# Kernel optimization log

Measured on AMD Instinct MI355X. Metric: run time of the kernel, lower is better.

## Reference

```python
import jax, jax.numpy as jnp
import numpy as np

B, L, D_IN = 8, 512, 1024
HEAD_SIZE = 64
NUM_LABELS = 16
INF = 1e12


def _rotary_sin_cos(seq_len, dim):
    # HF RoFormerSinusoidalPositionalEmbedding: inv_freq = 10000^(-2i/dim)
    pos = np.arange(seq_len, dtype=np.float64)[:, None]
    inv_freq = 1.0 / np.power(10000.0, 2.0 * np.arange(dim // 2) / dim)
    ang = pos * inv_freq  # [L, dim//2]
    # interleave: [s0, s0, s1, s1, ...] (matches stack([sin,sin],-1).reshape)
    sin = jnp.asarray(np.repeat(np.sin(ang), 2, axis=-1), dtype=jnp.float32)
    cos = jnp.asarray(np.repeat(np.cos(ang), 2, axis=-1), dtype=jnp.float32)
    return sin[None], cos[None]  # [1, L, dim]


def _rotate_half(x):
    # [-x1, x0, -x3, x2, ...]
    return jnp.stack([-x[..., 1::2], x[..., ::2]], axis=-1).reshape(x.shape)


def setup_inputs() -> dict:
    key = jax.random.key(0)
    k1, k2, k3, k4, k5 = jax.random.split(key, 5)
    s1 = 1.0 / np.sqrt(D_IN)
    s2 = 1.0 / np.sqrt(2 * HEAD_SIZE)
    return {
        "inputs": jax.random.normal(k1, (B, L, D_IN), dtype=jnp.float32),
        "attention_mask": jnp.ones((B, L), dtype=jnp.int32),
        "W1": jax.random.uniform(k2, (D_IN, 2 * HEAD_SIZE), jnp.float32, -s1, s1),
        "b1": jax.random.uniform(k3, (2 * HEAD_SIZE,), jnp.float32, -s1, s1),
        "W2": jax.random.uniform(k4, (2 * HEAD_SIZE, 2 * NUM_LABELS), jnp.float32, -s2, s2),
        "b2": jax.random.uniform(k5, (2 * NUM_LABELS,), jnp.float32, -s2, s2),
    }


def reference(inputs, attention_mask, W1, b1, W2, b2):
    h = inputs @ W1 + b1                      # [B, L, 2*head_size]
    qw, kw = h[..., ::2], h[..., 1::2]        # [B, L, head_size]

    sin, cos = _rotary_sin_cos(h.shape[1], HEAD_SIZE)
    qw = qw * cos + _rotate_half(qw) * sin
    kw = kw * cos + _rotate_half(kw) * sin

    logits = jnp.einsum("bmd,bnd->bmn", qw, kw) / (HEAD_SIZE ** 0.5)  # [B, L, L]

    bias = (h @ W2 + b2).transpose(0, 2, 1) / 2.0        # [B, 2*heads, L]
    logits = logits[:, None] + bias[:, ::2, None, :] + bias[:, 1::2, :, None]  # [B, heads, L, L]

    am = attention_mask.astype(logits.dtype)
    attn_mask = 1.0 - am[:, None, None, :] * am[:, None, :, None]
    logits = logits - attn_mask * INF

    tril = jnp.tril(jnp.ones((h.shape[1], h.shape[1]), logits.dtype), k=-1)
    logits = logits - tril * INF
    return logits
```

## Files before the change

kernel.cpp:

```cpp
#include <hip/hip_runtime.h>
#include <math.h>

#define B_   8
#define L_   512
#define DIN  1024
#define H_   128
#define HEAD 64
#define NL   16
#define INF_ 1.0e12f

#define SIN_OFF  0
#define COS_OFF  (512*32)
#define QROT_OFF (COS_OFF + 512*32)
#define KROT_OFF (QROT_OFF + B_*L_*HEAD)
#define BQ_OFF   (KROT_OFF + B_*L_*HEAD)
#define BK_OFF   (BQ_OFF + B_*NL*L_)
#define W1T_OFF  (BK_OFF + B_*NL*L_)

#define XSH_STRIDE 1032

typedef float          floatx4  __attribute__((ext_vector_type(4)));
typedef short          shortx8  __attribute__((ext_vector_type(8)));
typedef unsigned short ushortx8 __attribute__((ext_vector_type(8)));

__device__ __forceinline__ unsigned short f2bf(float f) {
    unsigned u = __float_as_uint(f);
    u += 0x7FFFu + ((u >> 16) & 1u);
    return (unsigned short)(u >> 16);
}

__global__ __launch_bounds__(256) void prep_kernel(const float* __restrict__ W1,
                                                   float* __restrict__ ws) {
    __shared__ float lds[64 * 132];
    const int tid = threadIdx.x;
    const int bid = blockIdx.x;

    if (bid < 64) {
        int idx = bid * 256 + tid;
        int m = idx >> 5, i = idx & 31;
        float freq = expf(-(float)i * 0.28782313662425575f);
        float ang  = (float)m * freq;
        ws[SIN_OFF + idx] = sinf(ang);
        ws[COS_OFF + idx] = cosf(ang);
    } else {
        const int k0 = (bid - 64) * 64;
        for (int i = 0; i < 8; i++) {
            int f = tid + i * 256;
            int k = f >> 5, n4 = (f & 31) * 4;
            *(float4*)&lds[k * 132 + n4] = *(const float4*)&W1[(size_t)(k0 + k) * H_ + n4];
        }
        __syncthreads();
        unsigned short* W1T = (unsigned short*)(ws + W1T_OFF);
        const int n  = tid >> 1;
        const int kh = (tid & 1) * 32;
        for (int i = 0; i < 4; i++) {
            ushortx8 p;
            #pragma unroll
            for (int j = 0; j < 8; j++) p[j] = f2bf(lds[(kh + i * 8 + j) * 132 + n]);
            *(ushortx8*)&W1T[(size_t)n * DIN + k0 + kh + i * 8] = p;
        }
    }
}

__global__ __launch_bounds__(1024) void gemm1_fused_kernel(
    const float* __restrict__ X, const float* __restrict__ b1,
    const float* __restrict__ W2, const float* __restrict__ b2,
    float* __restrict__ ws)
{
    __shared__ __align__(16) float shbuf[8256];
    __shared__ float hs[16 * 132];
    __shared__ float W2s[4096];

    unsigned short* Xsh = (unsigned short*)shbuf;
    float (*red)[16][64] = (float(*)[16][64])shbuf;

    const int tid  = threadIdx.x;
    const int m0   = blockIdx.x * 16;
    const int w    = tid >> 6;
    const int g    = w & 3;
    const int s    = w >> 2;
    const int lane = tid & 63;
    const int lrow = lane >> 4;
    const int lcol = lane & 15;

    const unsigned short* W1T = (const unsigned short*)(ws + W1T_OFF);

    const float* xrow = X + (size_t)(m0 + w) * DIN + lane * 8;
    float4 x0 = *(const float4*)(xrow + 0);
    float4 x1 = *(const float4*)(xrow + 4);
    float4 x2 = *(const float4*)(xrow + 512);
    float4 x3 = *(const float4*)(xrow + 516);

    const unsigned short* pB0 = W1T + (size_t)(g * 32 + lcol) * DIN + s * 256 + lrow * 8;
    const unsigned short* pB1 = pB0 + (size_t)16 * DIN;
    shortx8 bfr[16];
    #pragma unroll
    for (int st = 0; st < 8; st++) {
        bfr[2 * st]     = *(const shortx8*)(pB0 + st * 32);
        bfr[2 * st + 1] = *(const shortx8*)(pB1 + st * 32);
    }

    ((float4*)W2s)[tid] = ((const float4*)W2)[tid];

    {
        ushortx8 ua, ub;
        ua[0] = f2bf(x0.x); ua[1] = f2bf(x0.y); ua[2] = f2bf(x0.z); ua[3] = f2bf(x0.w);
        ua[4] = f2bf(x1.x); ua[5] = f2bf(x1.y); ua[6] = f2bf(x1.z); ua[7] = f2bf(x1.w);
        ub[0] = f2bf(x2.x); ub[1] = f2bf(x2.y); ub[2] = f2bf(x2.z); ub[3] = f2bf(x2.w);
        ub[4] = f2bf(x3.x); ub[5] = f2bf(x3.y); ub[6] = f2bf(x3.z); ub[7] = f2bf(x3.w);
        *(ushortx8*)&Xsh[w * XSH_STRIDE + lane * 8]       = ua;
        *(ushortx8*)&Xsh[w * XSH_STRIDE + 512 + lane * 8] = ub;
    }
    __syncthreads();

    const unsigned short* pA = &Xsh[lcol * XSH_STRIDE + s * 256 + lrow * 8];

    floatx4 acc0 = {0.f, 0.f, 0.f, 0.f};
    floatx4 acc1 = {0.f, 0.f, 0.f, 0.f};

    #pragma unroll
    for (int st = 0; st < 8; st++) {
        shortx8 af = *(const shortx8*)(pA + st * 32);
        acc0 = __builtin_amdgcn_mfma_f32_16x16x32_bf16(af, bfr[2 * st],     acc0, 0, 0, 0);
        acc1 = __builtin_amdgcn_mfma_f32_16x16x32_bf16(af, bfr[2 * st + 1], acc1, 0, 0, 0);
    }
    __syncthreads();

    #pragma unroll
    for (int r = 0; r < 4; r++) {
        red[r][w][lane]     = acc0[r];
        red[4 + r][w][lane] = acc1[r];
    }
    __syncthreads();

    if (w < 4) {
        float b1a = b1[g * 32 + lcol];
        float b1b = b1[g * 32 + 16 + lcol];
        #pragma unroll
        for (int r = 0; r < 4; r++) {
            float v0 = red[r][g][lane]     + red[r][g + 4][lane]
                     + red[r][g + 8][lane] + red[r][g + 12][lane];
            float v1 = red[4 + r][g][lane]     + red[4 + r][g + 4][lane]
                     + red[4 + r][g + 8][lane] + red[4 + r][g + 12][lane];
            hs[(lrow * 4 + r) * 132 + g * 32 + lcol]      = v0 + b1a;
            hs[(lrow * 4 + r) * 132 + g * 32 + 16 + lcol] = v1 + b1b;
        }
    }
    __syncthreads();

    if (tid < 256) {
        int row = tid >> 4;
        int j   = tid & 15;
        int gg  = m0 + row;
        int pos = gg & (L_ - 1);
        const float* hr = &hs[row * 132];
        float h0 = hr[8 * j + 0], h1 = hr[8 * j + 1];
        float h2 = hr[8 * j + 2], h3 = hr[8 * j + 3];
        float h4 = hr[8 * j + 4], h5 = hr[8 * j + 5];
        float h6 = hr[8 * j + 6], h7 = hr[8 * j + 7];
        float s0 = ws[SIN_OFF + pos * 32 + 2 * j];
        float c0 = ws[COS_OFF + pos * 32 + 2 * j];
        float s1 = ws[SIN_OFF + pos * 32 + 2 * j + 1];
        float c1 = ws[COS_OFF + pos * 32 + 2 * j + 1];
        float4 q, k;
        q.x = h0 * c0 - h2 * s0;  q.y = h2 * c0 + h0 * s0;
        q.z = h4 * c1 - h6 * s1;  q.w = h6 * c1 + h4 * s1;
        k.x = h1 * c0 - h3 * s0;  k.y = h3 * c0 + h1 * s0;
        k.z = h5 * c1 - h7 * s1;  k.w = h7 * c1 + h5 * s1;
        *(float4*)&ws[QROT_OFF + (size_t)gg * HEAD + 4 * j] = q;
        *(float4*)&ws[KROT_OFF + (size_t)gg * HEAD + 4 * j] = k;
    } else if (tid < 768) {
        int idx = tid - 256;
        int row = idx >> 5;
        int o   = idx & 31;
        float sum = b2[o];
        const float* hr = &hs[row * 132];
        #pragma unroll
        for (int c = 0; c < H_; c += 4) {
            sum += hr[c + 0] * W2s[(c + 0) * 32 + o]
                 + hr[c + 1] * W2s[(c + 1) * 32 + o]
                 + hr[c + 2] * W2s[(c + 2) * 32 + o]
                 + hr[c + 3] * W2s[(c + 3) * 32 + o];
        }
        sum *= 0.5f;
        int gg  = m0 + row;
        int bb  = gg >> 9;
        int pos = gg & (L_ - 1);
        if (o & 1) ws[BQ_OFF + ((size_t)bb * NL + (o >> 1)) * L_ + pos] = sum;
        else       ws[BK_OFF + ((size_t)bb * NL + (o >> 1)) * L_ + pos] = sum;
    }
}

__global__ __launch_bounds__(256) void qk_bcast_kernel(
    const int* __restrict__ am, const float* __restrict__ ws, float* __restrict__ out)
{
    __shared__ float Qs[64][68];
    __shared__ float Ks[64][68];
    __shared__ float BQs[16][64];
    __shared__ float BKs[16][64];
    __shared__ float maskM[64];
    __shared__ float maskN[64];

    const int tid = threadIdx.x;
    const int bid = blockIdx.x;
    const int bb = bid >> 6;
    const int mt = (bid >> 3) & 7;
    const int nt = bid & 7;
    const int m0 = mt * 64, n0 = nt * 64;

    {
        int r0   = tid >> 4;
        int dcol = (tid & 15) * 4;
        #pragma unroll
        for (int rr = 0; rr < 4; rr++) {
            int r = r0 + rr * 16;
            float4 q = *(const float4*)&ws[QROT_OFF + ((size_t)(bb * L_ + m0 + r)) * HEAD + dcol];
            float4 k = *(const float4*)&ws[KROT_OFF + ((size_t)(bb * L_ + n0 + r)) * HEAD + dcol];
            Qs[dcol + 0][r] = q.x; Qs[dcol + 1][r] = q.y;
            Qs[dcol + 2][r] = q.z; Qs[dcol + 3][r] = q.w;
            Ks[dcol + 0][r] = k.x; Ks[dcol + 1][r] = k.y;
            Ks[dcol + 2][r] = k.z; Ks[dcol + 3][r] = k.w;
        }
    }
    {
        int l = tid >> 4;
        int c = (tid & 15) * 4;
        *(float4*)&BQs[l][c] = *(const float4*)&ws[BQ_OFF + ((size_t)bb * NL + l) * L_ + m0 + c];
        *(float4*)&BKs[l][c] = *(const float4*)&ws[BK_OFF + ((size_t)bb * NL + l) * L_ + n0 + c];
    }
    if (tid < 64)       maskM[tid]      = (float)am[bb * L_ + m0 + tid];
    else if (tid < 128) maskN[tid - 64] = (float)am[bb * L_ + n0 + (tid - 64)];
    __syncthreads();

    const int ty = tid >> 4;
    const int tx = tid & 15;
    float acc[4][4] = {};
    #pragma unroll 8
    for (int d = 0; d < HEAD; d++) {
        float4 a  = *(const float4*)&Qs[d][ty * 4];
        float4 bv = *(const float4*)&Ks[d][tx * 4];
        acc[0][0] += a.x * bv.x; acc[0][1] += a.x * bv.y; acc[0][2] += a.x * bv.z; acc[0][3] += a.x * bv.w;
        acc[1][0] += a.y * bv.x; acc[1][1] += a.y * bv.y; acc[1][2] += a.y * bv.z; acc[1][3] += a.y * bv.w;
        acc[2][0] += a.z * bv.x; acc[2][1] += a.z * bv.y; acc[2][2] += a.z * bv.z; acc[2][3] += a.z * bv.w;
        acc[3][0] += a.w * bv.x; acc[3][1] += a.w * bv.y; acc[3][2] += a.w * bv.z; acc[3][3] += a.w * bv.w;
    }

    float4 base[4];
    #pragma unroll
    for (int r = 0; r < 4; r++) {
        int m = m0 + ty * 4 + r;
        float mm = maskM[ty * 4 + r];
        #pragma unroll
        for (int c = 0; c < 4; c++) {
            int n = n0 + tx * 4 + c;
            float v = acc[r][c] * 0.125f
                    - (1.0f - mm * maskN[tx * 4 + c]) * INF_
                    - ((n < m) ? INF_ : 0.0f);
            ((float*)&base[r])[c] = v;
        }
    }

    #pragma unroll
    for (int l = 0; l < NL; l++) {
        float4 bk4 = *(const float4*)&BKs[l][tx * 4];
        size_t outb = (((size_t)(bb * NL + l)) * L_ + m0 + ty * 4) * L_ + n0 + tx * 4;
        #pragma unroll
        for (int r = 0; r < 4; r++) {
            float bq = BQs[l][ty * 4 + r];
            float4 o;
            o.x = base[r].x + bk4.x + bq;
            o.y = base[r].y + bk4.y + bq;
            o.z = base[r].z + bk4.z + bq;
            o.w = base[r].w + bk4.w + bq;
            *(float4*)&out[outb + (size_t)r * L_] = o;
        }
    }
}

extern "C" void kernel_launch(void* const* d_in, const int* in_sizes, int n_in,
                              void* d_out, int out_size, void* d_ws, size_t ws_size,
                              hipStream_t stream) {
    const float* X  = (const float*)d_in[0];
    const int*   am = (const int*)d_in[1];
    const float* W1 = (const float*)d_in[2];
    const float* b1 = (const float*)d_in[3];
    const float* W2 = (const float*)d_in[4];
    const float* b2 = (const float*)d_in[5];
    float* out = (float*)d_out;
    float* ws  = (float*)d_ws;

    prep_kernel<<<80, 256, 0, stream>>>(W1, ws);
    gemm1_fused_kernel<<<(B_ * L_) / 16, 1024, 0, stream>>>(X, b1, W2, b2, ws);
    qk_bcast_kernel<<<B_ * (L_ / 64) * (L_ / 64), 256, 0, stream>>>(am, ws, out);
}
```

Measured before the change: 49.22 us.

## Restructure gemm1 to 8-row blocks with per-wave full-K MFMA and B prefetch

The fused projection kernel now processes 8 rows per 512-thread block instead of 16 rows per 1024 threads. Each wave owns 16 output columns and covers the full K dimension, which removes the split-K LDS reduction and one barrier. W1 fragments are loaded in double-buffered register batches interleaved with the MFMAs. Half of each 16-row MFMA tile is wasted because only 8 real rows exist (rows are duplicated via lcol&7), and twice as many blocks reload W2 and W1 data.

```diff
diff --git a/kernel.cpp b/kernel.cpp
--- a/kernel.cpp
+++ b/kernel.cpp
@@ -62,45 +62,55 @@
     }
 }
 
-__global__ __launch_bounds__(1024) void gemm1_fused_kernel(
+
+#define LOADB(b0,b1,b2,b3,b4,b5,b6,b7, kb) \
+    b0 = *(const shortx8*)(pB + (kb + 0) * 32); \
+    b1 = *(const shortx8*)(pB + (kb + 1) * 32); \
+    b2 = *(const shortx8*)(pB + (kb + 2) * 32); \
+    b3 = *(const shortx8*)(pB + (kb + 3) * 32); \
+    b4 = *(const shortx8*)(pB + (kb + 4) * 32); \
+    b5 = *(const shortx8*)(pB + (kb + 5) * 32); \
+    b6 = *(const shortx8*)(pB + (kb + 6) * 32); \
+    b7 = *(const shortx8*)(pB + (kb + 7) * 32); \
+    asm volatile("" :: "v"(b0), "v"(b1), "v"(b2), "v"(b3), \
+                       "v"(b4), "v"(b5), "v"(b6), "v"(b7));
+
+#define MFMA8(b0,b1,b2,b3,b4,b5,b6,b7, kb) \
+    acc = __builtin_amdgcn_mfma_f32_16x16x32_bf16(*(const shortx8*)(pA + (kb + 0) * 32), b0, acc, 0, 0, 0); \
+    acc = __builtin_amdgcn_mfma_f32_16x16x32_bf16(*(const shortx8*)(pA + (kb + 1) * 32), b1, acc, 0, 0, 0); \
+    acc = __builtin_amdgcn_mfma_f32_16x16x32_bf16(*(const shortx8*)(pA + (kb + 2) * 32), b2, acc, 0, 0, 0); \
+    acc = __builtin_amdgcn_mfma_f32_16x16x32_bf16(*(const shortx8*)(pA + (kb + 3) * 32), b3, acc, 0, 0, 0); \
+    acc = __builtin_amdgcn_mfma_f32_16x16x32_bf16(*(const shortx8*)(pA + (kb + 4) * 32), b4, acc, 0, 0, 0); \
+    acc = __builtin_amdgcn_mfma_f32_16x16x32_bf16(*(const shortx8*)(pA + (kb + 5) * 32), b5, acc, 0, 0, 0); \
+    acc = __builtin_amdgcn_mfma_f32_16x16x32_bf16(*(const shortx8*)(pA + (kb + 6) * 32), b6, acc, 0, 0, 0); \
+    acc = __builtin_amdgcn_mfma_f32_16x16x32_bf16(*(const shortx8*)(pA + (kb + 7) * 32), b7, acc, 0, 0, 0);
+
+__global__ __launch_bounds__(512) void gemm1_fused_kernel(
     const float* __restrict__ X, const float* __restrict__ b1,
     const float* __restrict__ W2, const float* __restrict__ b2,
     float* __restrict__ ws)
 {
-    __shared__ __align__(16) float shbuf[8256];
-    __shared__ float hs[16 * 132];
+    __shared__ __align__(16) unsigned short Xsh[8 * XSH_STRIDE];
+    __shared__ float hs[8 * 132];
     __shared__ float W2s[4096];
 
-    unsigned short* Xsh = (unsigned short*)shbuf;
-    float (*red)[16][64] = (float(*)[16][64])shbuf;
-
     const int tid  = threadIdx.x;
-    const int m0   = blockIdx.x * 16;
+    const int m0   = blockIdx.x * 8;
     const int w    = tid >> 6;
-    const int g    = w & 3;
-    const int s    = w >> 2;
     const int lane = tid & 63;
     const int lrow = lane >> 4;
     const int lcol = lane & 15;
 
     const unsigned short* W1T = (const unsigned short*)(ws + W1T_OFF);
 
-    const float* xrow = X + (size_t)(m0 + w) * DIN + lane * 8;
+    const float* xrow = X + (size_t)(m0 + w) * DIN + lane * 16;
     float4 x0 = *(const float4*)(xrow + 0);
     float4 x1 = *(const float4*)(xrow + 4);
-    float4 x2 = *(const float4*)(xrow + 512);
-    float4 x3 = *(const float4*)(xrow + 516);
-
-    const unsigned short* pB0 = W1T + (size_t)(g * 32 + lcol) * DIN + s * 256 + lrow * 8;
-    const unsigned short* pB1 = pB0 + (size_t)16 * DIN;
-    shortx8 bfr[16];
-    #pragma unroll
-    for (int st = 0; st < 8; st++) {
-        bfr[2 * st]     = *(const shortx8*)(pB0 + st * 32);
-        bfr[2 * st + 1] = *(const shortx8*)(pB1 + st * 32);
-    }
-
-    ((float4*)W2s)[tid] = ((const float4*)W2)[tid];
+    float4 x2 = *(const float4*)(xrow + 8);
+    float4 x3 = *(const float4*)(xrow + 12);
+
+    ((float4*)W2s)[tid]       = ((const float4*)W2)[tid];
+    ((float4*)W2s)[tid + 512] = ((const float4*)W2)[tid + 512];
 
     {
         ushortx8 ua, ub;
@@ -108,47 +118,37 @@
         ua[4] = f2bf(x1.x); ua[5] = f2bf(x1.y); ua[6] = f2bf(x1.z); ua[7] = f2bf(x1.w);
         ub[0] = f2bf(x2.x); ub[1] = f2bf(x2.y); ub[2] = f2bf(x2.z); ub[3] = f2bf(x2.w);
         ub[4] = f2bf(x3.x); ub[5] = f2bf(x3.y); ub[6] = f2bf(x3.z); ub[7] = f2bf(x3.w);
-        *(ushortx8*)&Xsh[w * XSH_STRIDE + lane * 8]       = ua;
-        *(ushortx8*)&Xsh[w * XSH_STRIDE + 512 + lane * 8] = ub;
-    }
+        *(ushortx8*)&Xsh[w * XSH_STRIDE + lane * 16]     = ua;
+        *(ushortx8*)&Xsh[w * XSH_STRIDE + lane * 16 + 8] = ub;
+    }
+
+    const unsigned short* pB = W1T + (size_t)(w * 16 + lcol) * DIN + lrow * 8;
+    shortx8 a0, a1, a2, a3, a4, a5, a6, a7;
+    shortx8 c0, c1, c2, c3, c4, c5, c6, c7;
+
+    LOADB(a0,a1,a2,a3,a4,a5,a6,a7, 0)
     __syncthreads();
 
-    const unsigned short* pA = &Xsh[lcol * XSH_STRIDE + s * 256 + lrow * 8];
-
-    floatx4 acc0 = {0.f, 0.f, 0.f, 0.f};
-    floatx4 acc1 = {0.f, 0.f, 0.f, 0.f};
-
-    #pragma unroll
-    for (int st = 0; st < 8; st++) {
-        shortx8 af = *(const shortx8*)(pA + st * 32);
-        acc0 = __builtin_amdgcn_mfma_f32_16x16x32_bf16(af, bfr[2 * st],     acc0, 0, 0, 0);
-        acc1 = __builtin_amdgcn_mfma_f32_16x16x32_bf16(af, bfr[2 * st + 1], acc1, 0, 0, 0);
+    const unsigned short* pA = &Xsh[(lcol & 7) * XSH_STRIDE + lrow * 8];
+    floatx4 acc = {0.f, 0.f, 0.f, 0.f};
+
+    LOADB(c0,c1,c2,c3,c4,c5,c6,c7, 8)
+    MFMA8(a0,a1,a2,a3,a4,a5,a6,a7, 0)
+    LOADB(a0,a1,a2,a3,a4,a5,a6,a7, 16)
+    MFMA8(c0,c1,c2,c3,c4,c5,c6,c7, 8)
+    LOADB(c0,c1,c2,c3,c4,c5,c6,c7, 24)
+    MFMA8(a0,a1,a2,a3,a4,a5,a6,a7, 16)
+    MFMA8(c0,c1,c2,c3,c4,c5,c6,c7, 24)
+
+    if (lrow < 2) {
+        float b1v = b1[w * 16 + lcol];
+        #pragma unroll
+        for (int r = 0; r < 4; r++)
+            hs[(lrow * 4 + r) * 132 + w * 16 + lcol] = acc[r] + b1v;
     }
     __syncthreads();
 
-    #pragma unroll
-    for (int r = 0; r < 4; r++) {
-        red[r][w][lane]     = acc0[r];
-        red[4 + r][w][lane] = acc1[r];
-    }
-    __syncthreads();
-
-    if (w < 4) {
-        float b1a = b1[g * 32 + lcol];
-        float b1b = b1[g * 32 + 16 + lcol];
-        #pragma unroll
-        for (int r = 0; r < 4; r++) {
-            float v0 = red[r][g][lane]     + red[r][g + 4][lane]
-                     + red[r][g + 8][lane] + red[r][g + 12][lane];
-            float v1 = red[4 + r][g][lane]     + red[4 + r][g + 4][lane]
-                     + red[4 + r][g + 8][lane] + red[4 + r][g + 12][lane];
-            hs[(lrow * 4 + r) * 132 + g * 32 + lcol]      = v0 + b1a;
-            hs[(lrow * 4 + r) * 132 + g * 32 + 16 + lcol] = v1 + b1b;
-        }
-    }
-    __syncthreads();
-
-    if (tid < 256) {
+    if (tid < 128) {
         int row = tid >> 4;
         int j   = tid & 15;
         int gg  = m0 + row;
@@ -159,18 +159,18 @@
         float h4 = hr[8 * j + 4], h5 = hr[8 * j + 5];
         float h6 = hr[8 * j + 6], h7 = hr[8 * j + 7];
         float s0 = ws[SIN_OFF + pos * 32 + 2 * j];
-        float c0 = ws[COS_OFF + pos * 32 + 2 * j];
+        float c0f = ws[COS_OFF + pos * 32 + 2 * j];
         float s1 = ws[SIN_OFF + pos * 32 + 2 * j + 1];
-        float c1 = ws[COS_OFF + pos * 32 + 2 * j + 1];
+        float c1f = ws[COS_OFF + pos * 32 + 2 * j + 1];
         float4 q, k;
-        q.x = h0 * c0 - h2 * s0;  q.y = h2 * c0 + h0 * s0;
-        q.z = h4 * c1 - h6 * s1;  q.w = h6 * c1 + h4 * s1;
-        k.x = h1 * c0 - h3 * s0;  k.y = h3 * c0 + h1 * s0;
-        k.z = h5 * c1 - h7 * s1;  k.w = h7 * c1 + h5 * s1;
+        q.x = h0 * c0f - h2 * s0;  q.y = h2 * c0f + h0 * s0;
+        q.z = h4 * c1f - h6 * s1;  q.w = h6 * c1f + h4 * s1;
+        k.x = h1 * c0f - h3 * s0;  k.y = h3 * c0f + h1 * s0;
+        k.z = h5 * c1f - h7 * s1;  k.w = h7 * c1f + h5 * s1;
         *(float4*)&ws[QROT_OFF + (size_t)gg * HEAD + 4 * j] = q;
         *(float4*)&ws[KROT_OFF + (size_t)gg * HEAD + 4 * j] = k;
-    } else if (tid < 768) {
-        int idx = tid - 256;
+    } else if (tid < 384) {
+        int idx = tid - 128;
         int row = idx >> 5;
         int o   = idx & 31;
         float sum = b2[o];
@@ -290,6 +290,6 @@
     float* ws  = (float*)d_ws;
 
     prep_kernel<<<80, 256, 0, stream>>>(W1, ws);
-    gemm1_fused_kernel<<<(B_ * L_) / 16, 1024, 0, stream>>>(X, b1, W2, b2, ws);
+    gemm1_fused_kernel<<<(B_ * L_) / 8, 512, 0, stream>>>(X, b1, W2, b2, ws);
     qk_bcast_kernel<<<B_ * (L_ / 64) * (L_ / 64), 256, 0, stream>>>(am, ws, out);
 }
```

Result: slower. 56.54 us (+14.9%).
